# Kernel optimization log

Hardware: AMD Instinct MI355X
Metric: run time of the kernel (lower is better)

The kernel has to match this reference:

```python
import jax, jax.numpy as jnp
import numpy as np

N_SIM = 2
EPS = 1e-8


def _masked_topk_cosine(embeddings):
    """VxV cosine similarity -> relu -> keep top-N_SIM per row -> row-normalize.
    Matches WeightedCrossEntropyLoss's on-the-fly similarity construction
    (neg_sim=False, normalize_sim=True, empty stop_idx)."""
    V = embeddings.shape[0]
    norms = jnp.linalg.norm(embeddings, axis=1, keepdims=True)  # [V,1]
    sims = (embeddings @ embeddings.T) / jnp.maximum(norms * norms.T, EPS)  # [V,V]
    sims = jnp.maximum(sims, 0.0)  # relu (neg_sim=False)
    _, idx = jax.lax.top_k(sims, N_SIM)  # [V,N_SIM]
    mask = jnp.zeros((V, V), dtype=sims.dtype).at[jnp.arange(V)[:, None], idx].set(1.0)
    sims = sims * mask
    sims = sims / jnp.sum(sims, axis=1, keepdims=True)  # normalize_sim=True
    return sims


def setup_inputs() -> dict:
    key = jax.random.key(0)
    k1, k2, k3 = jax.random.split(key, 3)
    B, V, D = 8192, 16384, 512
    output = jax.random.normal(k1, (B, V), dtype=jnp.float32)
    targets = jax.random.randint(k2, (B,), 0, V, dtype=jnp.int64 if jax.config.jax_enable_x64 else jnp.int32)
    embeddings = jax.random.normal(k3, (V, D), dtype=jnp.float32)
    return {"output": output, "targets": targets, "embeddings": embeddings}


def reference(output, targets, embeddings):
    sims = jax.lax.stop_gradient(_masked_topk_cosine(embeddings))  # torch.no_grad()
    log_probs = jax.nn.log_softmax(output, axis=1)  # [B,V]
    loss = jnp.mean(jnp.sum(-log_probs * sims[targets], axis=1))
    return loss
```

## Files before the change

kernel.cpp:

```cpp
#include <hip/hip_runtime.h>
#include <hip/hip_bf16.h>
#include <stdint.h>

#define VV 16384
#define DD 512
#define BB 8192

typedef __attribute__((ext_vector_type(8))) short short8;
typedef __attribute__((ext_vector_type(4))) float f32x4;

__device__ __forceinline__ void async_copy16(const void* g, void* l) {
  __builtin_amdgcn_global_load_lds(
      (const __attribute__((address_space(1))) char*)g,
      (__attribute__((address_space(3))) char*)l, 16, 0, 0);
}

__global__ __launch_bounds__(256) void k_normalize(
    const float* __restrict__ emb, __hip_bfloat16* __restrict__ ebf,
    unsigned long long* __restrict__ slots, float* __restrict__ loss) {
  const int row = blockIdx.x;
  const int tid = threadIdx.x;
  const float2 x = ((const float2*)(emb + (size_t)row * DD))[tid];
  float ss = x.x * x.x + x.y * x.y;
  for (int off = 32; off; off >>= 1) ss += __shfl_down(ss, off);
  __shared__ float red[4];
  __shared__ float rn_s;
  if ((tid & 63) == 0) red[tid >> 6] = ss;
  __syncthreads();
  if (tid == 0) rn_s = rsqrtf(red[0] + red[1] + red[2] + red[3]);
  __syncthreads();
  const float rn = rn_s;
  __hip_bfloat162 v;
  v.x = __float2bfloat16(x.x * rn);
  v.y = __float2bfloat16(x.y * rn);
  ((__hip_bfloat162*)ebf)[(size_t)row * (DD / 2) + tid] = v;
  if (tid == 0) {
    slots[row] = 0ull;
    if (row == 0) *loss = 0.f;
  }
}

__global__ __launch_bounds__(256) void k_simargmax(
    const __hip_bfloat16* __restrict__ ebf,
    unsigned long long* __restrict__ slots) {
  __shared__ __align__(16) char ldsA[128 * 64];
  __shared__ __align__(16) char ldsB[128 * 64];
  const int tid  = threadIdx.x;
  const int wv   = tid >> 6;
  const int lane = tid & 63;
  const int q    = lane >> 4;
  const int ln   = lane & 15;
  const int rowBase = blockIdx.y * 128;
  const int colBase = blockIdx.x * 128;
  const char* gA = (const char*)ebf + (size_t)rowBase * (DD * 2);
  const char* gB = (const char*)ebf + (size_t)colBase * (DD * 2);
  const int r0   = tid >> 2;
  const int koff = (tid & 3) * 16;

  f32x4 acc[4][4];
#pragma unroll
  for (int i = 0; i < 4; i++)
#pragma unroll
    for (int j = 0; j < 4; j++) acc[i][j] = (f32x4){0.f, 0.f, 0.f, 0.f};

  char* lA = ldsA + wv * 1024;
  char* lB = ldsB + wv * 1024;
  const int wrow = (wv >> 1) * 64;
  const int wcol = (wv & 1) * 64;

  for (int kk = 0; kk < DD * 2; kk += 64) {
    const char* a = gA + (size_t)r0 * (DD * 2) + kk + koff;
    const char* b = gB + (size_t)r0 * (DD * 2) + kk + koff;
    async_copy16(a, lA);
    async_copy16(a + 64 * (DD * 2), lA + 4096);
    async_copy16(b, lB);
    async_copy16(b + 64 * (DD * 2), lB + 4096);
    __syncthreads();

    short8 af[4], bf[4];
#pragma unroll
    for (int i = 0; i < 4; i++)
      af[i] = *(const short8*)(ldsA + (wrow + i * 16 + ln) * 64 + q * 16);
#pragma unroll
    for (int j = 0; j < 4; j++)
      bf[j] = *(const short8*)(ldsB + (wcol + j * 16 + ln) * 64 + q * 16);
#pragma unroll
    for (int i = 0; i < 4; i++)
#pragma unroll
      for (int j = 0; j < 4; j++)
        acc[i][j] = __builtin_amdgcn_mfma_f32_16x16x32_bf16(af[i], bf[j],
                                                            acc[i][j], 0, 0, 0);
    __syncthreads();
  }

#pragma unroll
  for (int i = 0; i < 4; i++) {
#pragma unroll
    for (int r = 0; r < 4; r++) {
      const int R = rowBase + wrow + i * 16 + q * 4 + r;
      unsigned long long best = 0ull;
#pragma unroll
      for (int j = 0; j < 4; j++) {
        const int C = colBase + wcol + j * 16 + ln;
        float v = acc[i][j][r];
        v = (C == R) ? 0.f : fmaxf(v, 0.f);
        unsigned long long pv =
            ((unsigned long long)__float_as_uint(v) << 32) | (unsigned)C;
        best = pv > best ? pv : best;
      }
      for (int m = 1; m < 16; m <<= 1) {
        unsigned long long o = __shfl_xor(best, m, 64);
        best = o > best ? o : best;
      }
      if (ln == 0) atomicMax(&slots[R], best);
    }
  }
}

__global__ __launch_bounds__(256) void k_loss(
    const float* __restrict__ out, const int* __restrict__ targets,
    const unsigned long long* __restrict__ slots, float* __restrict__ loss) {
  const int b = blockIdx.x;
  const int tid = threadIdx.x;
  const float* row = out + (size_t)b * VV;
  float s = 0.f;
#pragma unroll
  for (int i = 0; i < VV / 256; i++) s += __expf(row[tid + i * 256]);
  for (int off = 32; off; off >>= 1) s += __shfl_down(s, off);
  __shared__ float red[4];
  if ((tid & 63) == 0) red[tid >> 6] = s;
  __syncthreads();
  if (tid == 0) {
    const float lse = __logf(red[0] + red[1] + red[2] + red[3]);
    const int t = targets[b];
    const unsigned long long pv = slots[t];
    const float sv = __uint_as_float((unsigned)(pv >> 32));
    const int j = (int)(pv & 0xffffffffu);
    const float w1 = sv / (1.f + sv);
    const float w0 = 1.f - w1;
    const float lb = lse - w0 * row[t] - w1 * row[j];
    atomicAdd(loss, lb * (1.f / (float)BB));
  }
}

extern "C" void kernel_launch(void* const* d_in, const int* in_sizes, int n_in,
                              void* d_out, int out_size, void* d_ws,
                              size_t ws_size, hipStream_t stream) {
  (void)in_sizes; (void)n_in; (void)out_size; (void)ws_size;
  const float* output  = (const float*)d_in[0];
  const int*   targets = (const int*)d_in[1];
  const float* emb     = (const float*)d_in[2];
  float* loss = (float*)d_out;
  __hip_bfloat16* ebf = (__hip_bfloat16*)d_ws;
  unsigned long long* slots =
      (unsigned long long*)((char*)d_ws + (size_t)VV * DD * 2);

  hipLaunchKernelGGL(k_normalize, dim3(VV), dim3(256), 0, stream,
                     emb, ebf, slots, loss);
  hipLaunchKernelGGL(k_simargmax, dim3(VV / 128, VV / 128), dim3(256), 0,
                     stream, ebf, slots);
  hipLaunchKernelGGL(k_loss, dim3(BB), dim3(256), 0, stream,
                     output, targets, slots, loss);
}
```

Measured before the change: 1.197 ms.

## Compute similarity argmax only for target rows gathered per batch element

```diff
diff --git a/kernel.cpp b/kernel.cpp
--- a/kernel.cpp
+++ b/kernel.cpp
@@ -35,16 +35,17 @@
   v.y = __float2bfloat16(x.y * rn);
   ((__hip_bfloat162*)ebf)[(size_t)row * (DD / 2) + tid] = v;
   if (tid == 0) {
-    slots[row] = 0ull;
+    if (row < BB) slots[row] = 0ull;
     if (row == 0) *loss = 0.f;
   }
 }
 
 __global__ __launch_bounds__(256) void k_simargmax(
-    const __hip_bfloat16* __restrict__ ebf,
+    const __hip_bfloat16* __restrict__ ebf, const int* __restrict__ targets,
     unsigned long long* __restrict__ slots) {
   __shared__ __align__(16) char ldsA[128 * 64];
   __shared__ __align__(16) char ldsB[128 * 64];
+  __shared__ int tgt_s[128];
   const int tid  = threadIdx.x;
   const int wv   = tid >> 6;
   const int lane = tid & 63;
@@ -52,10 +53,13 @@
   const int ln   = lane & 15;
   const int rowBase = blockIdx.y * 128;
   const int colBase = blockIdx.x * 128;
-  const char* gA = (const char*)ebf + (size_t)rowBase * (DD * 2);
+  if (tid < 128) tgt_s[tid] = targets[rowBase + tid];
   const char* gB = (const char*)ebf + (size_t)colBase * (DD * 2);
   const int r0   = tid >> 2;
   const int koff = (tid & 3) * 16;
+  __syncthreads();
+  const size_t tA0 = (size_t)tgt_s[r0] * (DD * 2);
+  const size_t tA1 = (size_t)tgt_s[r0 + 64] * (DD * 2);
 
   f32x4 acc[4][4];
 #pragma unroll
@@ -69,10 +73,9 @@
   const int wcol = (wv & 1) * 64;
 
   for (int kk = 0; kk < DD * 2; kk += 64) {
-    const char* a = gA + (size_t)r0 * (DD * 2) + kk + koff;
+    async_copy16((const char*)ebf + tA0 + kk + koff, lA);
+    async_copy16((const char*)ebf + tA1 + kk + koff, lA + 4096);
     const char* b = gB + (size_t)r0 * (DD * 2) + kk + koff;
-    async_copy16(a, lA);
-    async_copy16(a + 64 * (DD * 2), lA + 4096);
     async_copy16(b, lB);
     async_copy16(b + 64 * (DD * 2), lB + 4096);
     __syncthreads();
@@ -97,13 +100,14 @@
   for (int i = 0; i < 4; i++) {
 #pragma unroll
     for (int r = 0; r < 4; r++) {
-      const int R = rowBase + wrow + i * 16 + q * 4 + r;
+      const int Rl = wrow + i * 16 + q * 4 + r;
+      const int tR = tgt_s[Rl];
       unsigned long long best = 0ull;
 #pragma unroll
       for (int j = 0; j < 4; j++) {
         const int C = colBase + wcol + j * 16 + ln;
         float v = acc[i][j][r];
-        v = (C == R) ? 0.f : fmaxf(v, 0.f);
+        v = (C == tR) ? 0.f : fmaxf(v, 0.f);
         unsigned long long pv =
             ((unsigned long long)__float_as_uint(v) << 32) | (unsigned)C;
         best = pv > best ? pv : best;
@@ -112,35 +116,49 @@
         unsigned long long o = __shfl_xor(best, m, 64);
         best = o > best ? o : best;
       }
-      if (ln == 0) atomicMax(&slots[R], best);
+      if (ln == 0) atomicMax(&slots[rowBase + Rl], best);
     }
   }
 }
 
-__global__ __launch_bounds__(256) void k_loss(
-    const float* __restrict__ out, const int* __restrict__ targets,
-    const unsigned long long* __restrict__ slots, float* __restrict__ loss) {
+__global__ __launch_bounds__(256) void k_lse(const float* __restrict__ out,
+                                             float* __restrict__ lse) {
   const int b = blockIdx.x;
   const int tid = threadIdx.x;
-  const float* row = out + (size_t)b * VV;
-  float s = 0.f;
+  const float4* row = (const float4*)(out + (size_t)b * VV);
+  float s0 = 0.f, s1 = 0.f, s2 = 0.f, s3 = 0.f;
 #pragma unroll
-  for (int i = 0; i < VV / 256; i++) s += __expf(row[tid + i * 256]);
+  for (int i = 0; i < VV / 1024; i++) {
+    const float4 v = row[tid + i * 256];
+    s0 += __expf(v.x); s1 += __expf(v.y); s2 += __expf(v.z); s3 += __expf(v.w);
+  }
+  float s = (s0 + s1) + (s2 + s3);
   for (int off = 32; off; off >>= 1) s += __shfl_down(s, off);
   __shared__ float red[4];
   if ((tid & 63) == 0) red[tid >> 6] = s;
   __syncthreads();
-  if (tid == 0) {
-    const float lse = __logf(red[0] + red[1] + red[2] + red[3]);
-    const int t = targets[b];
-    const unsigned long long pv = slots[t];
-    const float sv = __uint_as_float((unsigned)(pv >> 32));
-    const int j = (int)(pv & 0xffffffffu);
-    const float w1 = sv / (1.f + sv);
-    const float w0 = 1.f - w1;
-    const float lb = lse - w0 * row[t] - w1 * row[j];
-    atomicAdd(loss, lb * (1.f / (float)BB));
-  }
+  if (tid == 0) lse[b] = __logf(red[0] + red[1] + red[2] + red[3]);
+}
+
+__global__ __launch_bounds__(256) void k_final(
+    const float* __restrict__ out, const int* __restrict__ targets,
+    const unsigned long long* __restrict__ slots,
+    const float* __restrict__ lse, float* __restrict__ loss) {
+  const int tid = threadIdx.x;
+  const int b = blockIdx.x * 256 + tid;
+  const int t = targets[b];
+  const unsigned long long pv = slots[b];
+  const float sv = __uint_as_float((unsigned)(pv >> 32));
+  const int j = (int)(pv & 0xffffffffu);
+  const float w1 = sv / (1.f + sv);
+  const float w0 = 1.f - w1;
+  float lb = (lse[b] - w0 * out[(size_t)b * VV + t] -
+              w1 * out[(size_t)b * VV + j]) * (1.f / (float)BB);
+  for (int off = 32; off; off >>= 1) lb += __shfl_down(lb, off);
+  __shared__ float red[4];
+  if ((tid & 63) == 0) red[tid >> 6] = lb;
+  __syncthreads();
+  if (tid == 0) atomicAdd(loss, red[0] + red[1] + red[2] + red[3]);
 }
 
 extern "C" void kernel_launch(void* const* d_in, const int* in_sizes, int n_in,
@@ -151,14 +169,17 @@
   const int*   targets = (const int*)d_in[1];
   const float* emb     = (const float*)d_in[2];
   float* loss = (float*)d_out;
-  __hip_bfloat16* ebf = (__hip_bfloat16*)d_ws;
+  char* ws = (char*)d_ws;
+  __hip_bfloat16* ebf = (__hip_bfloat16*)ws;
   unsigned long long* slots =
-      (unsigned long long*)((char*)d_ws + (size_t)VV * DD * 2);
+      (unsigned long long*)(ws + (size_t)VV * DD * 2);
+  float* lse = (float*)(ws + (size_t)VV * DD * 2 + (size_t)BB * 8);
 
   hipLaunchKernelGGL(k_normalize, dim3(VV), dim3(256), 0, stream,
                      emb, ebf, slots, loss);
-  hipLaunchKernelGGL(k_simargmax, dim3(VV / 128, VV / 128), dim3(256), 0,
-                     stream, ebf, slots);
-  hipLaunchKernelGGL(k_loss, dim3(BB), dim3(256), 0, stream,
-                     output, targets, slots, loss);
+  hipLaunchKernelGGL(k_simargmax, dim3(VV / 128, BB / 128), dim3(256), 0,
+                     stream, ebf, targets, slots);
+  hipLaunchKernelGGL(k_lse, dim3(BB), dim3(256), 0, stream, output, lse);
+  hipLaunchKernelGGL(k_final, dim3(BB / 256), dim3(256), 0, stream,
+                     output, targets, slots, lse, loss);
 }
```

After: 1.014 ms. -15.3%, faster.
